# Performance work log

Measured on AMD Instinct MI355X. Metric: run time of the kernel, lower is better.

Reference implementation:

```python
import jax, jax.numpy as jnp
import numpy as np

N = 20000          # nodes
E = 320000         # edges
IN_C = 512         # input features
HID = 512          # 2*out_channels (first GCN layer width)
OUT = 256          # out_channels == num_hidden
PROJ = 256         # num_proj_hidden


def _gcn_conv(x, W, b, src, dst):
    """PyG GCNConv: x' = D^{-1/2}(A+I)D^{-1/2} X W + b (self-loops added)."""
    n = x.shape[0]
    x = x @ W  # [N, F_out]
    ones = jnp.ones((src.shape[0],), x.dtype)
    deg = jax.ops.segment_sum(ones, dst, num_segments=n) + 1.0  # +1 self-loop
    dis = jax.lax.rsqrt(deg)
    coef = dis[src] * dis[dst]                      # [E]
    agg = jax.ops.segment_sum(x[src] * coef[:, None], dst, num_segments=n)
    agg = agg + x * (dis * dis)[:, None]            # self-loop messages
    return agg + b


def setup_inputs() -> dict:
    key = jax.random.key(0)
    ks = jax.random.split(key, 12)
    s = 0.02
    return {
        "node_features": jax.random.normal(ks[0], (N, IN_C), jnp.float32),
        "edge_index": jax.random.randint(ks[1], (2, E), 0, N, jnp.int64),
        "W1": jax.random.normal(ks[2], (IN_C, HID), jnp.float32) * s,
        "b1": jnp.zeros((HID,), jnp.float32),
        "W2": jax.random.normal(ks[3], (HID, OUT), jnp.float32) * s,
        "b2": jnp.zeros((OUT,), jnp.float32),
        "a": jnp.asarray(0.25, jnp.float32),  # shared PReLU weight
        "W3": jax.random.normal(ks[4], (OUT, PROJ), jnp.float32) * s,
        "b3": jnp.zeros((PROJ,), jnp.float32),
        "W4": jax.random.normal(ks[5], (PROJ, OUT), jnp.float32) * s,
        "b4": jnp.zeros((OUT,), jnp.float32),
    }


def reference(node_features, edge_index, W1, b1, W2, b2, a, W3, b3, W4, b4):
    src, dst = edge_index[0], edge_index[1]
    prelu = lambda x: jnp.where(x > 0, x, a * x)
    h = prelu(_gcn_conv(node_features, W1, b1, src, dst))
    h = prelu(_gcn_conv(h, W2, b2, src, dst))
    # projection MLP: Linear -> ELU -> Linear
    h2 = jax.nn.elu(h @ W3 + b3)
    return h2 @ W4 + b4
```

## Files before the change

kernel.cpp:

```cpp
#include <hip/hip_runtime.h>
#include <stdint.h>

typedef unsigned short u16;
typedef unsigned int   u32;
typedef __attribute__((ext_vector_type(8))) short short8;
typedef __attribute__((ext_vector_type(4))) float f32x4;

__device__ __forceinline__ float bf2f(u16 h){
    return __uint_as_float(((u32)h) << 16);
}
__device__ __forceinline__ u16 f2bf(float f){
    u32 u = __float_as_uint(f);
    u += 0x7fffu + ((u >> 16) & 1u);
    return (u16)(u >> 16);
}

__device__ __forceinline__ void gl_lds16(const void* g, void* l){
    __builtin_amdgcn_global_load_lds(
        (__attribute__((address_space(1))) void*)(uintptr_t)g,
        (__attribute__((address_space(3))) void*)(uintptr_t)l,
        16, 0, 0);
}

__device__ __forceinline__ int probe_fmt(const int* ei, int* sh){
    int t = threadIdx.x & 255;
    if (threadIdx.x == 0) *sh = 0;
    __syncthreads();
    if (threadIdx.x < 256 && ei[2*t + 1] != 0) atomicOr(sh, 1);
    __syncthreads();
    return *sh;
}
__device__ __forceinline__ int eload(const int* ei, int fmt, int idx){
    return fmt ? ei[idx] : ei[2*idx];
}

#define CAP 96
__global__ void scatter(const int* __restrict__ ei, int* __restrict__ cnt,
                        int* __restrict__ buck, int E, int N){
    __shared__ int sh;
    int fmt = probe_fmt(ei, &sh);
    int e = blockIdx.x * 256 + threadIdx.x;
    if (e < E){
        int d = eload(ei, fmt, E + e);
        if ((unsigned)d < (unsigned)N){
            int slot = atomicAdd(&cnt[d], 1);
            if (slot < CAP) buck[(size_t)d * CAP + slot] = eload(ei, fmt, e);
        }
    }
}

__global__ void transpose_x(const void* w1, const void* w2, const void* w3,
                            const void* w4, const void* X,
                            const void* b1, const void* b2, const void* b3,
                            const void* b4, const void* av,
                            u16* o1, u16* o2, u16* o3, u16* o4,
                            u16* xbf, u16* d1, u16* d2, u16* d3, u16* d4,
                            u16* da, int NN){
    __shared__ int sf;
    __shared__ u16 tb[32][33];
    int lt = threadIdx.y * 32 + threadIdx.x;
    if (lt == 0) sf = 0;
    __syncthreads();
    {
        int huge = 0;
        const u16* w = (const u16*)w1;
        #pragma unroll
        for (int k = 0; k < 8; k++){
            u16 h = w[lt * 8 + k];
            if (((h >> 7) & 0xFF) >= 0x7F) huge = 1;
        }
        if (huge) atomicOr(&sf, 1);
    }
    __syncthreads();
    int f32 = sf;

    if (blockIdx.z == 4){
        #define CV(s,i) (f32 ? f2bf(((const float*)(s))[i]) : ((const u16*)(s))[i])
        if (blockIdx.x == 0 && blockIdx.y == 0){
            d1[lt]       = CV(b1, lt);
            d1[lt + 256] = CV(b1, lt + 256);
            d2[lt] = CV(b2, lt);
            d3[lt] = CV(b3, lt);
            d4[lt] = CV(b4, lt);
            if (lt == 0) da[0] = CV(av, 0);
        }
        #undef CV
        size_t nb8 = (size_t)NN * 64;
        size_t step = 256u * 256u;
        for (size_t i = (size_t)(blockIdx.y * 16 + blockIdx.x) * 256 + lt; i < nb8; i += step){
            short8 o;
            if (f32){
                const float* p = (const float*)X + i * 8;
                f32x4 a0 = *(const f32x4*)p;
                f32x4 a1 = *(const f32x4*)(p + 4);
                #pragma unroll
                for (int j = 0; j < 4; j++){
                    o[j]     = (short)f2bf(a0[j]);
                    o[4 + j] = (short)f2bf(a1[j]);
                }
            } else {
                o = *(const short8*)((const u16*)X + i * 8);
            }
            *(short8*)(xbf + i * 8) = o;
        }
        return;
    }

    const void* in; u16* out; int K, N;
    switch (blockIdx.z){
        case 0:  in = w1; out = o1; K = 512; N = 512; break;
        case 1:  in = w2; out = o2; K = 512; N = 256; break;
        case 2:  in = w3; out = o3; K = 256; N = 256; break;
        default: in = w4; out = o4; K = 256; N = 256; break;
    }
    int bx = blockIdx.x * 32;
    int by = blockIdx.y * 32;
    if (bx >= N || by >= K) return;
    int x = threadIdx.x, y = threadIdx.y;
    #pragma unroll
    for (int i = 0; i < 32; i += 8){
        size_t idx = (size_t)(by + y + i) * N + bx + x;
        tb[y + i][x] = f32 ? f2bf(((const float*)in)[idx]) : ((const u16*)in)[idx];
    }
    __syncthreads();
    #pragma unroll
    for (int i = 0; i < 32; i += 8)
        out[(size_t)(bx + y + i) * K + by + x] = tb[x][y + i];
}

#define GTN 128
#define GBK 64

template<int MODE, int OUTF>
__global__ __launch_bounds__(256) void gemm128(
    const u16* __restrict__ A, const u16* __restrict__ BT,
    const u16* __restrict__ bias, void* __restrict__ Cv,
    int M, int K, int N, int nN)
{
    __shared__ __align__(16) u16 As[128 * GBK];
    __shared__ __align__(16) u16 Bs[GTN * GBK];
    int nwg = gridDim.x;
    int flat = blockIdx.x;
    int q8 = nwg >> 3, r8 = nwg & 7;
    int xcd = flat & 7, idx8 = flat >> 3;
    int wg = (xcd < r8 ? xcd * (q8 + 1) : r8 * (q8 + 1) + (xcd - r8) * q8) + idx8;
    int bm = (wg / nN) * 128;
    int bn = (wg % nN) * GTN;

    int tid  = threadIdx.x;
    int lane = tid & 63;
    int wm   = (tid >> 7) & 1;
    int wn   = (tid >> 6) & 1;

    f32x4 acc[4][4] = {};

    int srow = tid >> 3;
    int scol = (tid & 7) * 8;
    const u16* aP = A  + (size_t)(bm + srow) * K + scol;
    const u16* bP = BT + (size_t)(bn + srow) * K + scol;
    u16* lA = &As[tid * 8];
    u16* lB = &Bs[tid * 8];

    int q   = lane >> 4;
    int r16 = lane & 15;
    const u16* ra = &As[(wm*64 + r16) * GBK + q*8];
    const u16* rb = &Bs[(wn*64 + r16) * GBK + q*8];

    for (int k0 = 0; k0 < K; k0 += GBK){
        #pragma unroll
        for (int r = 0; r < 4; r++){
            gl_lds16(aP + (size_t)r*32*K + k0, lA + r*32*GBK);
            gl_lds16(bP + (size_t)r*32*K + k0, lB + r*32*GBK);
        }
        __syncthreads();
        #pragma unroll
        for (int kk = 0; kk < 2; kk++){
            short8 af[4], bf[4];
            #pragma unroll
            for (int i = 0; i < 4; i++) af[i] = *(const short8*)(ra + i*16*GBK + kk*32);
            #pragma unroll
            for (int j = 0; j < 4; j++) bf[j] = *(const short8*)(rb + j*16*GBK + kk*32);
            #pragma unroll
            for (int i = 0; i < 4; i++)
                #pragma unroll
                for (int j = 0; j < 4; j++)
                    acc[i][j] = __builtin_amdgcn_mfma_f32_16x16x32_bf16(af[i], bf[j], acc[i][j], 0, 0, 0);
        }
        __syncthreads();
    }

    int q4 = q * 4;
    #pragma unroll
    for (int i = 0; i < 4; i++){
        #pragma unroll
        for (int j = 0; j < 4; j++){
            int gcol = bn + wn*64 + j*16 + r16;
            float bvv = (MODE >= 1) ? bf2f(bias[gcol]) : 0.f;
            #pragma unroll
            for (int r = 0; r < 4; r++){
                int grow = bm + wm*64 + i*16 + q4 + r;
                if (grow < M){
                    float v = acc[i][j][r] + bvv;
                    if (MODE == 2) v = (v > 0.f) ? v : expm1f(v);
                    if (OUTF) ((float*)Cv)[(size_t)grow * N + gcol] = v;
                    else      ((u16*)Cv)[(size_t)grow * N + gcol] = f2bf(v);
                }
            }
        }
    }
}

__global__ __launch_bounds__(256) void gemm34(
    const u16* __restrict__ Q, const u16* __restrict__ W3T,
    const u16* __restrict__ W4T, const u16* __restrict__ b3,
    const u16* __restrict__ b4, float* __restrict__ OUT, int M)
{
    __shared__ __align__(16) u16 As[64 * 64];
    __shared__ __align__(16) u16 Bs[256 * 64];
    __shared__ __align__(16) u16 T[64 * 256];
    int nwg = gridDim.x;
    int flat = blockIdx.x;
    int q8 = nwg >> 3, r8 = nwg & 7;
    int xcd = flat & 7, idx8 = flat >> 3;
    int wg = (xcd < r8 ? xcd * (q8 + 1) : r8 * (q8 + 1) + (xcd - r8) * q8) + idx8;
    int bm = wg * 64;

    int tid  = threadIdx.x;
    int lane = tid & 63;
    int wm   = (tid >> 7) & 1;
    int wn   = (tid >> 6) & 1;
    int q    = lane >> 4;
    int r16  = lane & 15;
    int q4   = q * 4;
    int srow = tid >> 3;
    int scol = (tid & 7) * 8;

    u16* lA = &As[tid * 8];
    u16* lB = &Bs[tid * 8];
    const u16* ra = &As[(wm*32 + r16) * 64 + q*8];
    const u16* rb = &Bs[(wn*128 + r16) * 64 + q*8];

    f32x4 acc[2][8];

    #pragma unroll
    for (int i = 0; i < 2; i++)
        #pragma unroll
        for (int j = 0; j < 8; j++) acc[i][j] = (f32x4){0,0,0,0};
    {
        const u16* aP = Q   + (size_t)(bm + srow) * 256 + scol;
        const u16* bP = W3T + (size_t)srow * 256 + scol;
        for (int ks = 0; ks < 4; ks++){
            int k0 = ks * 64;
            #pragma unroll
            for (int r = 0; r < 2; r++)
                gl_lds16(aP + (size_t)r*32*256 + k0, lA + r*32*64);
            #pragma unroll
            for (int r = 0; r < 8; r++)
                gl_lds16(bP + (size_t)r*32*256 + k0, lB + r*32*64);
            __syncthreads();
            #pragma unroll
            for (int kk = 0; kk < 2; kk++){
                short8 af[2], bf[8];
                #pragma unroll
                for (int i = 0; i < 2; i++) af[i] = *(const short8*)(ra + i*16*64 + kk*32);
                #pragma unroll
                for (int j = 0; j < 8; j++) bf[j] = *(const short8*)(rb + j*16*64 + kk*32);
                #pragma unroll
                for (int i = 0; i < 2; i++)
                    #pragma unroll
                    for (int j = 0; j < 8; j++)
                        acc[i][j] = __builtin_amdgcn_mfma_f32_16x16x32_bf16(af[i], bf[j], acc[i][j], 0, 0, 0);
            }
            __syncthreads();
        }
    }
    #pragma unroll
    for (int i = 0; i < 2; i++){
        #pragma unroll
        for (int j = 0; j < 8; j++){
            int lc = wn*128 + j*16 + r16;
            float bvv = bf2f(b3[lc]);
            #pragma unroll
            for (int r = 0; r < 4; r++){
                int lr = wm*32 + i*16 + q4 + r;
                float v = acc[i][j][r] + bvv;
                v = (v > 0.f) ? v : expm1f(v);
                T[lr * 256 + lc] = f2bf(v);
            }
        }
    }
    __syncthreads();

    #pragma unroll
    for (int i = 0; i < 2; i++)
        #pragma unroll
        for (int j = 0; j < 8; j++) acc[i][j] = (f32x4){0,0,0,0};
    {
        const u16* bP = W4T + (size_t)srow * 256 + scol;
        for (int ks = 0; ks < 4; ks++){
            int k0 = ks * 64;
            #pragma unroll
            for (int r = 0; r < 8; r++)
                gl_lds16(bP + (size_t)r*32*256 + k0, lB + r*32*64);
            __syncthreads();
            #pragma unroll
            for (int kk = 0; kk < 2; kk++){
                short8 af[2], bf[8];
                #pragma unroll
                for (int i = 0; i < 2; i++)
                    af[i] = *(const short8*)&T[(wm*32 + i*16 + r16) * 256 + k0 + kk*32 + q*8];
                #pragma unroll
                for (int j = 0; j < 8; j++) bf[j] = *(const short8*)(rb + j*16*64 + kk*32);
                #pragma unroll
                for (int i = 0; i < 2; i++)
                    #pragma unroll
                    for (int j = 0; j < 8; j++)
                        acc[i][j] = __builtin_amdgcn_mfma_f32_16x16x32_bf16(af[i], bf[j], acc[i][j], 0, 0, 0);
            }
            __syncthreads();
        }
    }
    #pragma unroll
    for (int i = 0; i < 2; i++){
        #pragma unroll
        for (int j = 0; j < 8; j++){
            int lc = wn*128 + j*16 + r16;
            float bvv = bf2f(b4[lc]);
            #pragma unroll
            for (int r = 0; r < 4; r++){
                int grow = bm + wm*32 + i*16 + q4 + r;
                if (grow < M)
                    OUT[(size_t)grow * 256 + lc] = acc[i][j][r] + bvv;
            }
        }
    }
}

template<int F, int CH>
__global__ __launch_bounds__(256) void agg_b(
    const u16* __restrict__ XW, const int* __restrict__ cnt,
    const int* __restrict__ buck, const u16* __restrict__ bias,
    const u16* __restrict__ aptr, u16* __restrict__ out, int N)
{
    constexpr int NCH = F / CH;
    constexpr int LPN = CH / 8;
    constexpr int NPB = 256 / LPN;
    int bid = blockIdx.x;
    int chunk = bid % NCH;
    int node = (bid / NCH) * NPB + ((int)threadIdx.x >> 3);
    if (node >= N) return;
    int tf = chunk * CH + ((int)threadIdx.x & (LPN - 1)) * 8;
    float a  = bf2f(aptr[0]);
    int dgc = cnt[node];
    float di = rsqrtf((float)dgc + 1.0f);
    int deg = dgc < CAP ? dgc : CAP;
    const int* bk = buck + (size_t)node * CAP;
    float acc[8] = {0,0,0,0,0,0,0,0};
    int ng = (deg + 7) >> 3;
    int si[8]; float ci[8];
    if (ng > 0){
        #pragma unroll
        for (int u = 0; u < 8; u++){ int e = u < deg ? u : deg - 1; si[u] = bk[e]; }
        #pragma unroll
        for (int u = 0; u < 8; u++){
            float c = rsqrtf((float)cnt[si[u]] + 1.0f);
            ci[u] = (u < deg) ? c : 0.f;
        }
    }
    for (int g = 0; g < ng; g++){
        short8 vi[8];
        #pragma unroll
        for (int u = 0; u < 8; u++)
            vi[u] = *(const short8*)(XW + (size_t)si[u] * F + tf);
        int sn[8]; float cn[8];
        bool more = (g + 1) < ng;
        if (more){
            int base = (g + 1) * 8;
            #pragma unroll
            for (int u = 0; u < 8; u++){ int e = base + u; e = e < deg ? e : deg - 1; sn[u] = bk[e]; }
            #pragma unroll
            for (int u = 0; u < 8; u++){
                float c = rsqrtf((float)cnt[sn[u]] + 1.0f);
                cn[u] = (base + u < deg) ? c : 0.f;
            }
        }
        #pragma unroll
        for (int u = 0; u < 8; u++)
            #pragma unroll
            for (int j = 0; j < 8; j++)
                acc[j] += ci[u] * bf2f((u16)vi[u][j]);
        if (more){
            #pragma unroll
            for (int u = 0; u < 8; u++){ si[u] = sn[u]; ci[u] = cn[u]; }
        }
    }
    {
        short8 v = *(const short8*)(XW + (size_t)node * F + tf);
        #pragma unroll
        for (int j = 0; j < 8; j++) acc[j] += di * bf2f((u16)v[j]);
    }
    short8 bv = *(const short8*)(bias + tf);
    short8 o;
    #pragma unroll
    for (int j = 0; j < 8; j++){
        float x = di * acc[j] + bf2f((u16)bv[j]);
        x = (x > 0.f) ? x : a * x;
        o[j] = (short)f2bf(x);
    }
    *(short8*)(out + (size_t)node * F + tf) = o;
}

extern "C" void kernel_launch(void* const* d_in, const int* in_sizes, int n_in,
                              void* d_out, int out_size, void* d_ws, size_t ws_size,
                              hipStream_t stream)
{
    int iX=0, iEI=1, iW1=2, ib1=3, iW2=4, ib2=5, ia=6, iW3=7, ib3=8, iW4=9, ib4=10;
    {
        int jX=-1,jEI=-1,jW1=-1,jb1=-1,jW2=-1,ja=-1,jW3=-1,jW4=-1,jb2=-1,jb3=-1,jb4=-1;
        int n64k=0, n256=0;
        for (int i = 0; i < n_in; i++){
            switch (in_sizes[i]){
                case 10240000: jX = i; break;
                case 640000:   jEI = i; break;
                case 262144:   jW1 = i; break;
                case 131072:   jW2 = i; break;
                case 512:      jb1 = i; break;
                case 1:        ja = i; break;
                case 65536:    if (n64k++ == 0) jW3 = i; else jW4 = i; break;
                case 256: {
                    int k = n256++;
                    if (k == 0) jb2 = i; else if (k == 1) jb3 = i; else jb4 = i;
                } break;
                default: break;
            }
        }
        if (jX>=0&&jEI>=0&&jW1>=0&&jb1>=0&&jW2>=0&&ja>=0&&jW3>=0&&jW4>=0&&jb2>=0&&jb3>=0&&jb4>=0){
            iX=jX; iEI=jEI; iW1=jW1; ib1=jb1; iW2=jW2; ib2=jb2; ia=ja; iW3=jW3; ib3=jb3; iW4=jW4; ib4=jb4;
        }
    }
    int N = in_sizes[iX] / 512;
    int E = in_sizes[iEI] / 2;
    const int* EI = (const int*)d_in[iEI];
    float* OUT = (float*)d_out;
    u16*   S   = (u16*)d_out;

    char* ws = (char*)d_ws;
    size_t off = 0;
    auto alloc = [&](size_t bytes)->char*{
        char* p = ws + off;
        off = (off + bytes + 255) & ~(size_t)255;
        return p;
    };
    int MP = N + 128;
    int*   cnt  = (int*)  alloc((size_t)N*4);
    int*   buck = (int*)  alloc((size_t)N*CAP*4);
    u16*   WT1  = (u16*)  alloc((size_t)512*512*2);
    u16*   WT2  = (u16*)  alloc((size_t)256*512*2);
    u16*   WT3  = (u16*)  alloc((size_t)256*256*2);
    u16*   WT4  = (u16*)  alloc((size_t)256*256*2);
    u16*   b1c  = (u16*)  alloc((size_t)512*2);
    u16*   b2c  = (u16*)  alloc((size_t)256*2);
    u16*   b3c  = (u16*)  alloc((size_t)256*2);
    u16*   b4c  = (u16*)  alloc((size_t)256*2);
    u16*   ac   = (u16*)  alloc((size_t)8*2);
    u16*   Xbf  = (u16*)  alloc((size_t)MP*512*2);
    u16*   h1   = (u16*)  alloc((size_t)MP*512*2);
    u16*   P    = (u16*)  alloc((size_t)MP*256*2);
    u16*   Q    = (u16*)  alloc((size_t)MP*256*2);
    if (ws_size < off) return;

    hipMemsetAsync(cnt, 0, (size_t)N*4, stream);

    transpose_x<<<dim3(16, 16, 5), dim3(32, 8), 0, stream>>>(
        d_in[iW1], d_in[iW2], d_in[iW3], d_in[iW4], d_in[iX],
        d_in[ib1], d_in[ib2], d_in[ib3], d_in[ib4], d_in[ia],
        WT1, WT2, WT3, WT4, Xbf, b1c, b2c, b3c, b4c, ac, N);

    scatter<<<(E + 255)/256, 256, 0, stream>>>(EI, cnt, buck, E, N);

    int gm128 = (N + 127) / 128;
    int gm64  = (N + 63) / 64;
    int nodeb = (N + 31) / 32;

    gemm128<0,0><<<gm128*4, 256, 0, stream>>>(Xbf, WT1, nullptr, S, N, 512, 512, 4);
    agg_b<512,64><<<nodeb*8, 256, 0, stream>>>(S, cnt, buck, b1c, ac, h1, N);

    gemm128<0,0><<<gm128*2, 256, 0, stream>>>(h1, WT2, nullptr, P, N, 512, 256, 2);
    agg_b<256,64><<<nodeb*4, 256, 0, stream>>>(P, cnt, buck, b2c, ac, Q, N);

    gemm34<<<gm64, 256, 0, stream>>>(Q, WT3, WT4, b3c, b4c, OUT, N);
}
```

Before: 270.0 us.

## Fuse edge scatter into prep kernel and precompute degree norms in GEMM

The edge bucketing scatter moves into the weight/feature conversion kernel as an extra z-slice, which removes one launch. The first GEMM now also computes the per-node inverse-sqrt degree into a new buffer, so the aggregation kernels load a float instead of loading the count and computing rsqrt for every neighbour. The aggregation kernel also gets a launch-bounds occupancy hint. The fused scatter uses a fixed grid-stride loop and runs concurrently with the transposes, so its atomic traffic may compete with the conversion work.

```diff
diff --git a/kernel.cpp b/kernel.cpp
--- a/kernel.cpp
+++ b/kernel.cpp
@@ -22,43 +22,37 @@
         16, 0, 0);
 }
 
-__device__ __forceinline__ int probe_fmt(const int* ei, int* sh){
-    int t = threadIdx.x & 255;
-    if (threadIdx.x == 0) *sh = 0;
-    __syncthreads();
-    if (threadIdx.x < 256 && ei[2*t + 1] != 0) atomicOr(sh, 1);
-    __syncthreads();
-    return *sh;
-}
-__device__ __forceinline__ int eload(const int* ei, int fmt, int idx){
-    return fmt ? ei[idx] : ei[2*idx];
-}
-
 #define CAP 96
-__global__ void scatter(const int* __restrict__ ei, int* __restrict__ cnt,
-                        int* __restrict__ buck, int E, int N){
-    __shared__ int sh;
-    int fmt = probe_fmt(ei, &sh);
-    int e = blockIdx.x * 256 + threadIdx.x;
-    if (e < E){
-        int d = eload(ei, fmt, E + e);
-        if ((unsigned)d < (unsigned)N){
-            int slot = atomicAdd(&cnt[d], 1);
-            if (slot < CAP) buck[(size_t)d * CAP + slot] = eload(ei, fmt, e);
-        }
-    }
-}
-
-__global__ void transpose_x(const void* w1, const void* w2, const void* w3,
-                            const void* w4, const void* X,
-                            const void* b1, const void* b2, const void* b3,
-                            const void* b4, const void* av,
-                            u16* o1, u16* o2, u16* o3, u16* o4,
-                            u16* xbf, u16* d1, u16* d2, u16* d3, u16* d4,
-                            u16* da, int NN){
+
+__global__ void prep_all(const void* w1, const void* w2, const void* w3,
+                         const void* w4, const void* X,
+                         const void* b1, const void* b2, const void* b3,
+                         const void* b4, const void* av,
+                         const int* __restrict__ EI, int* __restrict__ cnt,
+                         int* __restrict__ buck, int E,
+                         u16* o1, u16* o2, u16* o3, u16* o4,
+                         u16* xbf, u16* d1, u16* d2, u16* d3, u16* d4,
+                         u16* da, int NN){
     __shared__ int sf;
     __shared__ u16 tb[32][33];
     int lt = threadIdx.y * 32 + threadIdx.x;
+
+    if (blockIdx.z == 5){
+        if (lt == 0) sf = 0;
+        __syncthreads();
+        if (EI[2*lt + 1] != 0) atomicOr(&sf, 1);
+        __syncthreads();
+        int fmt = sf;
+        for (int e = (blockIdx.y * 16 + blockIdx.x) * 256 + lt; e < E; e += 65536){
+            int d = fmt ? EI[E + e] : EI[2*(E + e)];
+            if ((unsigned)d < (unsigned)NN){
+                int slot = atomicAdd(&cnt[d], 1);
+                if (slot < CAP) buck[(size_t)d * CAP + slot] = fmt ? EI[e] : EI[2*e];
+            }
+        }
+        return;
+    }
+
     if (lt == 0) sf = 0;
     __syncthreads();
     {
@@ -135,10 +129,15 @@
 __global__ __launch_bounds__(256) void gemm128(
     const u16* __restrict__ A, const u16* __restrict__ BT,
     const u16* __restrict__ bias, void* __restrict__ Cv,
-    int M, int K, int N, int nN)
+    int M, int K, int N, int nN,
+    const int* __restrict__ cntp, float* __restrict__ disp)
 {
     __shared__ __align__(16) u16 As[128 * GBK];
     __shared__ __align__(16) u16 Bs[GTN * GBK];
+    if (cntp){
+        for (int i = blockIdx.x * 256 + (int)threadIdx.x; i < M; i += gridDim.x * 256)
+            disp[i] = rsqrtf((float)cntp[i] + 1.0f);
+    }
     int nwg = gridDim.x;
     int flat = blockIdx.x;
     int q8 = nwg >> 3, r8 = nwg & 7;
@@ -337,10 +336,11 @@
 }
 
 template<int F, int CH>
-__global__ __launch_bounds__(256) void agg_b(
-    const u16* __restrict__ XW, const int* __restrict__ cnt,
-    const int* __restrict__ buck, const u16* __restrict__ bias,
-    const u16* __restrict__ aptr, u16* __restrict__ out, int N)
+__global__ __launch_bounds__(256, 8) void agg_b(
+    const u16* __restrict__ XW, const float* __restrict__ dis,
+    const int* __restrict__ cnt, const int* __restrict__ buck,
+    const u16* __restrict__ bias, const u16* __restrict__ aptr,
+    u16* __restrict__ out, int N)
 {
     constexpr int NCH = F / CH;
     constexpr int LPN = CH / 8;
@@ -351,8 +351,8 @@
     if (node >= N) return;
     int tf = chunk * CH + ((int)threadIdx.x & (LPN - 1)) * 8;
     float a  = bf2f(aptr[0]);
+    float di = dis[node];
     int dgc = cnt[node];
-    float di = rsqrtf((float)dgc + 1.0f);
     int deg = dgc < CAP ? dgc : CAP;
     const int* bk = buck + (size_t)node * CAP;
     float acc[8] = {0,0,0,0,0,0,0,0};
@@ -363,7 +363,7 @@
         for (int u = 0; u < 8; u++){ int e = u < deg ? u : deg - 1; si[u] = bk[e]; }
         #pragma unroll
         for (int u = 0; u < 8; u++){
-            float c = rsqrtf((float)cnt[si[u]] + 1.0f);
+            float c = dis[si[u]];
             ci[u] = (u < deg) ? c : 0.f;
         }
     }
@@ -380,7 +380,7 @@
             for (int u = 0; u < 8; u++){ int e = base + u; e = e < deg ? e : deg - 1; sn[u] = bk[e]; }
             #pragma unroll
             for (int u = 0; u < 8; u++){
-                float c = rsqrtf((float)cnt[sn[u]] + 1.0f);
+                float c = dis[sn[u]];
                 cn[u] = (base + u < deg) ? c : 0.f;
             }
         }
@@ -453,6 +453,7 @@
     };
     int MP = N + 128;
     int*   cnt  = (int*)  alloc((size_t)N*4);
+    float* dis  = (float*)alloc((size_t)N*4);
     int*   buck = (int*)  alloc((size_t)N*CAP*4);
     u16*   WT1  = (u16*)  alloc((size_t)512*512*2);
     u16*   WT2  = (u16*)  alloc((size_t)256*512*2);
@@ -471,22 +472,21 @@
 
     hipMemsetAsync(cnt, 0, (size_t)N*4, stream);
 
-    transpose_x<<<dim3(16, 16, 5), dim3(32, 8), 0, stream>>>(
+    prep_all<<<dim3(16, 16, 6), dim3(32, 8), 0, stream>>>(
         d_in[iW1], d_in[iW2], d_in[iW3], d_in[iW4], d_in[iX],
         d_in[ib1], d_in[ib2], d_in[ib3], d_in[ib4], d_in[ia],
+        EI, cnt, buck, E,
         WT1, WT2, WT3, WT4, Xbf, b1c, b2c, b3c, b4c, ac, N);
-
-    scatter<<<(E + 255)/256, 256, 0, stream>>>(EI, cnt, buck, E, N);
 
     int gm128 = (N + 127) / 128;
     int gm64  = (N + 63) / 64;
     int nodeb = (N + 31) / 32;
 
-    gemm128<0,0><<<gm128*4, 256, 0, stream>>>(Xbf, WT1, nullptr, S, N, 512, 512, 4);
-    agg_b<512,64><<<nodeb*8, 256, 0, stream>>>(S, cnt, buck, b1c, ac, h1, N);
-
-    gemm128<0,0><<<gm128*2, 256, 0, stream>>>(h1, WT2, nullptr, P, N, 512, 256, 2);
-    agg_b<256,64><<<nodeb*4, 256, 0, stream>>>(P, cnt, buck, b2c, ac, Q, N);
+    gemm128<0,0><<<gm128*4, 256, 0, stream>>>(Xbf, WT1, nullptr, S, N, 512, 512, 4, cnt, dis);
+    agg_b<512,64><<<nodeb*8, 256, 0, stream>>>(S, dis, cnt, buck, b1c, ac, h1, N);
+
+    gemm128<0,0><<<gm128*2, 256, 0, stream>>>(h1, WT2, nullptr, P, N, 512, 256, 2, nullptr, nullptr);
+    agg_b<256,64><<<nodeb*4, 256, 0, stream>>>(P, dis, cnt, buck, b2c, ac, Q, N);
 
     gemm34<<<gm64, 256, 0, stream>>>(Q, WT3, WT4, b3c, b4c, OUT, N);
 }
```

New measurement: 708.6 us. +162.4%, slower.
